# Kernel optimization log

Hardware: AMD Instinct MI355X
Metric: run time of the kernel (lower is better)

## Reference

```python
import jax, jax.numpy as jnp
import numpy as np

K = 512  # number of activations kept per row (init_kwargs k)


def setup_inputs() -> dict:
    key = jax.random.key(0)
    x = jax.random.normal(key, (8192, 8192), dtype=jnp.float32)
    return {"x": x}


def reference(x):
    # torch.topk(x, k, dim=1) -> indices of k largest per row
    _, idx = jax.lax.top_k(x, K)                      # idx: [B, K]
    rows = jnp.arange(x.shape[0])[:, None]            # [B, 1]
    # zeros_like + scatter(1, idx, 1)
    mask = jnp.zeros_like(x).at[rows, idx].set(1.0)   # [B, F]
    return x * mask
```

## Files before the change

### kernel.cpp

```cpp
#include <hip/hip_runtime.h>
#include <stdint.h>

#define FDIM 8192
#define KSEL 512
#define NT   512
#define EPT  (FDIM / NT / 4)

__device__ __forceinline__ unsigned keyOf(unsigned u) {
    return (u & 0x80000000u) ? ~u : (u | 0x80000000u);
}
__device__ __forceinline__ float valOf(unsigned key) {
    unsigned u = (key & 0x80000000u) ? (key ^ 0x80000000u) : ~key;
    return __uint_as_float(u);
}

__global__ __launch_bounds__(NT) void topk_mask_kernel(const float* __restrict__ x,
                                                       float* __restrict__ out) {
    __shared__ unsigned hist[256];
    __shared__ unsigned s_prefix, s_need, s_sub;
    __shared__ unsigned s_tiecnt;
    __shared__ unsigned tiebuf[64];

    const int row  = blockIdx.x;
    const int t    = threadIdx.x;
    const int lane = t & 63;

    const float4* xrow = (const float4*)(x + (size_t)row * FDIM);
    float4*       orow = (float4*)(out + (size_t)row * FDIM);

    uint4 kreg[EPT];
    #pragma unroll
    for (int j = 0; j < EPT; ++j) {
        float4 v = xrow[j * NT + t];
        kreg[j].x = keyOf(__float_as_uint(v.x));
        kreg[j].y = keyOf(__float_as_uint(v.y));
        kreg[j].z = keyOf(__float_as_uint(v.z));
        kreg[j].w = keyOf(__float_as_uint(v.w));
    }
    if (t < 256) hist[t] = 0u;
    if (t == 0) { s_prefix = 0u; s_need = KSEL; s_tiecnt = 0u; }
    __syncthreads();

    for (int round = 0; round < 4; ++round) {
        const int shift = 24 - 8 * round;
        const unsigned pref = s_prefix;

        if (round == 0) {
            #pragma unroll
            for (int j = 0; j < EPT; ++j) {
                #pragma unroll
                for (int c = 0; c < 4; ++c) {
                    unsigned key = (&kreg[j].x)[c];
                    unsigned dig = key >> 24;
                    unsigned long long m = ~0ull;
                    #pragma unroll
                    for (int b = 0; b < 8; ++b) {
                        unsigned long long bb = __ballot((dig >> b) & 1u);
                        m &= ((dig >> b) & 1u) ? bb : ~bb;
                    }
                    if (lane == __ffsll((long long)m) - 1)
                        atomicAdd(&hist[dig], (unsigned)__popcll(m));
                }
            }
        } else {
            #pragma unroll
            for (int j = 0; j < EPT; ++j) {
                #pragma unroll
                for (int c = 0; c < 4; ++c) {
                    unsigned key = (&kreg[j].x)[c];
                    if ((key >> (shift + 8)) == pref)
                        atomicAdd(&hist[(key >> shift) & 255u], 1u);
                }
            }
        }
        __syncthreads();

        if (t < 64) {
            const unsigned need = s_need;
            unsigned h0 = hist[4 * lane + 0];
            unsigned h1 = hist[4 * lane + 1];
            unsigned h2 = hist[4 * lane + 2];
            unsigned h3 = hist[4 * lane + 3];
            hist[4 * lane + 0] = 0u;
            hist[4 * lane + 1] = 0u;
            hist[4 * lane + 2] = 0u;
            hist[4 * lane + 3] = 0u;
            unsigned tot = h0 + h1 + h2 + h3;
            unsigned T = tot;
            #pragma unroll
            for (int off = 1; off < 64; off <<= 1) {
                unsigned y = __shfl_down(T, off);
                T += (lane + off < 64) ? y : 0u;
            }
            const unsigned beyond = T - tot;
            unsigned S3 = beyond + h3;
            unsigned S2 = S3 + h2;
            unsigned S1 = S2 + h1;
            unsigned S0 = S1 + h0;
            if (S0 >= need && S0 - h0 < need) {
                s_prefix = (pref << 8) | (unsigned)(4 * lane + 0);
                s_need = need - (S0 - h0); s_sub = h0;
            }
            if (S1 >= need && S1 - h1 < need) {
                s_prefix = (pref << 8) | (unsigned)(4 * lane + 1);
                s_need = need - (S1 - h1); s_sub = h1;
            }
            if (S2 >= need && S2 - h2 < need) {
                s_prefix = (pref << 8) | (unsigned)(4 * lane + 2);
                s_need = need - (S2 - h2); s_sub = h2;
            }
            if (S3 >= need && S3 - h3 < need) {
                s_prefix = (pref << 8) | (unsigned)(4 * lane + 3);
                s_need = need - (S3 - h3); s_sub = h3;
            }
        }
        __syncthreads();
    }

    const unsigned thresh = s_prefix;
    const unsigned keepEq = s_need;
    const unsigned eqCnt  = s_sub;
    const bool simple = (eqCnt == keepEq);

    if (simple) {
        #pragma unroll
        for (int j = 0; j < EPT; ++j) {
            uint4 k = kreg[j];
            float4 o;
            o.x = (k.x >= thresh) ? valOf(k.x) : 0.0f;
            o.y = (k.y >= thresh) ? valOf(k.y) : 0.0f;
            o.z = (k.z >= thresh) ? valOf(k.z) : 0.0f;
            o.w = (k.w >= thresh) ? valOf(k.w) : 0.0f;
            orow[j * NT + t] = o;
        }
    } else {
        #pragma unroll
        for (int j = 0; j < EPT; ++j) {
            uint4 k = kreg[j];
            float4 o;
            o.x = (k.x > thresh) ? valOf(k.x) : 0.0f;
            o.y = (k.y > thresh) ? valOf(k.y) : 0.0f;
            o.z = (k.z > thresh) ? valOf(k.z) : 0.0f;
            o.w = (k.w > thresh) ? valOf(k.w) : 0.0f;
            orow[j * NT + t] = o;
        }
        #pragma unroll
        for (int j = 0; j < EPT; ++j) {
            #pragma unroll
            for (int c = 0; c < 4; ++c) {
                unsigned key = (&kreg[j].x)[c];
                if (key == thresh) {
                    unsigned slot = atomicAdd(&s_tiecnt, 1u);
                    if (slot < 64u) tiebuf[slot] = 4u * (unsigned)(j * NT + t) + (unsigned)c;
                }
            }
        }
        __syncthreads();
        if (t == 0) {
            const unsigned m = s_tiecnt;
            const float v = valOf(thresh);
            if (m <= 64u) {
                for (unsigned i = 0; i < m; ++i) {
                    unsigned idx = tiebuf[i], rank = 0;
                    for (unsigned q = 0; q < m; ++q) rank += (tiebuf[q] < idx);
                    if (rank < keepEq) out[(size_t)row * FDIM + idx] = v;
                }
            } else {
                unsigned c = 0;
                for (int i = 0; i < FDIM && c < keepEq; ++i) {
                    if (keyOf(__float_as_uint(x[(size_t)row * FDIM + i])) == thresh) {
                        out[(size_t)row * FDIM + i] = v; ++c;
                    }
                }
            }
        }
    }
}

extern "C" void kernel_launch(void* const* d_in, const int* in_sizes, int n_in,
                              void* d_out, int out_size, void* d_ws, size_t ws_size,
                              hipStream_t stream) {
    const float* x = (const float*)d_in[0];
    float* out = (float*)d_out;
    topk_mask_kernel<<<dim3(FDIM), dim3(NT), 0, stream>>>(x, out);
}
```

Baseline: 455.4 us.

## Use 12/12/8-bit radix select with 4096-bin histogram and block-wide scan

Replaces the four 8-bit radix-select passes with three passes of 12, 12 and 8 bits, backed by a 4096-bin shared-memory histogram. The first pass drops the 8-ballot warp-aggregation loop and uses plain LDS atomics, relying on the wider bin spread to keep contention low. The threshold search becomes a scan across the whole block: per-thread suffix sums over 8 bins, a wave shuffle scan, then a cross-wave combine through shared memory. This removes a histogram pass and the ballot overhead, at the cost of more histogram zeroing, an extra barrier per round and 16KB of LDS.

```diff
diff --git a/kernel.cpp b/kernel.cpp
--- a/kernel.cpp
+++ b/kernel.cpp
@@ -5,6 +5,8 @@
 #define KSEL 512
 #define NT   512
 #define EPT  (FDIM / NT / 4)
+#define NBIN 4096
+#define NWAVE (NT / 64)
 
 __device__ __forceinline__ unsigned keyOf(unsigned u) {
     return (u & 0x80000000u) ? ~u : (u | 0x80000000u);
@@ -16,14 +18,15 @@
 
 __global__ __launch_bounds__(NT) void topk_mask_kernel(const float* __restrict__ x,
                                                        float* __restrict__ out) {
-    __shared__ unsigned hist[256];
-    __shared__ unsigned s_prefix, s_need, s_sub;
-    __shared__ unsigned s_tiecnt;
+    __shared__ unsigned hist[NBIN];
+    __shared__ unsigned wtot[NWAVE];
+    __shared__ unsigned s_prefix, s_need, s_sub, s_tiecnt;
     __shared__ unsigned tiebuf[64];
 
     const int row  = blockIdx.x;
     const int t    = threadIdx.x;
     const int lane = t & 63;
+    const int wave = t >> 6;
 
     const float4* xrow = (const float4*)(x + (size_t)row * FDIM);
     float4*       orow = (float4*)(out + (size_t)row * FDIM);
@@ -37,13 +40,15 @@
         kreg[j].z = keyOf(__float_as_uint(v.z));
         kreg[j].w = keyOf(__float_as_uint(v.w));
     }
-    if (t < 256) hist[t] = 0u;
+    #pragma unroll
+    for (int i = t; i < NBIN; i += NT) hist[i] = 0u;
     if (t == 0) { s_prefix = 0u; s_need = KSEL; s_tiecnt = 0u; }
     __syncthreads();
 
-    for (int round = 0; round < 4; ++round) {
-        const int shift = 24 - 8 * round;
+    #pragma unroll
+    for (int round = 0; round < 3; ++round) {
         const unsigned pref = s_prefix;
+        const unsigned need = s_need;
 
         if (round == 0) {
             #pragma unroll
@@ -51,15 +56,17 @@
                 #pragma unroll
                 for (int c = 0; c < 4; ++c) {
                     unsigned key = (&kreg[j].x)[c];
-                    unsigned dig = key >> 24;
-                    unsigned long long m = ~0ull;
-                    #pragma unroll
-                    for (int b = 0; b < 8; ++b) {
-                        unsigned long long bb = __ballot((dig >> b) & 1u);
-                        m &= ((dig >> b) & 1u) ? bb : ~bb;
-                    }
-                    if (lane == __ffsll((long long)m) - 1)
-                        atomicAdd(&hist[dig], (unsigned)__popcll(m));
+                    atomicAdd(&hist[key >> 20], 1u);
+                }
+            }
+        } else if (round == 1) {
+            #pragma unroll
+            for (int j = 0; j < EPT; ++j) {
+                #pragma unroll
+                for (int c = 0; c < 4; ++c) {
+                    unsigned key = (&kreg[j].x)[c];
+                    if ((key >> 20) == pref)
+                        atomicAdd(&hist[(key >> 8) & 0xFFFu], 1u);
                 }
             }
         } else {
@@ -68,50 +75,42 @@
                 #pragma unroll
                 for (int c = 0; c < 4; ++c) {
                     unsigned key = (&kreg[j].x)[c];
-                    if ((key >> (shift + 8)) == pref)
-                        atomicAdd(&hist[(key >> shift) & 255u], 1u);
+                    if ((key >> 8) == pref)
+                        atomicAdd(&hist[key & 0xFFu], 1u);
                 }
             }
         }
         __syncthreads();
 
-        if (t < 64) {
-            const unsigned need = s_need;
-            unsigned h0 = hist[4 * lane + 0];
-            unsigned h1 = hist[4 * lane + 1];
-            unsigned h2 = hist[4 * lane + 2];
-            unsigned h3 = hist[4 * lane + 3];
-            hist[4 * lane + 0] = 0u;
-            hist[4 * lane + 1] = 0u;
-            hist[4 * lane + 2] = 0u;
-            hist[4 * lane + 3] = 0u;
-            unsigned tot = h0 + h1 + h2 + h3;
-            unsigned T = tot;
-            #pragma unroll
-            for (int off = 1; off < 64; off <<= 1) {
-                unsigned y = __shfl_down(T, off);
-                T += (lane + off < 64) ? y : 0u;
-            }
-            const unsigned beyond = T - tot;
-            unsigned S3 = beyond + h3;
-            unsigned S2 = S3 + h2;
-            unsigned S1 = S2 + h1;
-            unsigned S0 = S1 + h0;
-            if (S0 >= need && S0 - h0 < need) {
-                s_prefix = (pref << 8) | (unsigned)(4 * lane + 0);
-                s_need = need - (S0 - h0); s_sub = h0;
-            }
-            if (S1 >= need && S1 - h1 < need) {
-                s_prefix = (pref << 8) | (unsigned)(4 * lane + 1);
-                s_need = need - (S1 - h1); s_sub = h1;
-            }
-            if (S2 >= need && S2 - h2 < need) {
-                s_prefix = (pref << 8) | (unsigned)(4 * lane + 2);
-                s_need = need - (S2 - h2); s_sub = h2;
-            }
-            if (S3 >= need && S3 - h3 < need) {
-                s_prefix = (pref << 8) | (unsigned)(4 * lane + 3);
-                s_need = need - (S3 - h3); s_sub = h3;
+        const unsigned base = (unsigned)t * (NBIN / NT);
+        unsigned sfx[9];
+        sfx[8] = 0u;
+        #pragma unroll
+        for (int i = 7; i >= 0; --i) sfx[i] = sfx[i + 1] + hist[base + i];
+        #pragma unroll
+        for (int i = 0; i < 8; ++i) hist[base + i] = 0u;
+        const unsigned tot = sfx[0];
+        unsigned incl = tot;
+        #pragma unroll
+        for (int off = 1; off < 64; off <<= 1) {
+            unsigned y = __shfl_down(incl, off);
+            incl += (lane + off < 64) ? y : 0u;
+        }
+        if (lane == 0) wtot[wave] = incl;
+        __syncthreads();
+        unsigned gb = incl - tot;
+        #pragma unroll
+        for (int w = 0; w < NWAVE; ++w) gb += (w > wave) ? wtot[w] : 0u;
+
+        #pragma unroll
+        for (int i = 0; i < 8; ++i) {
+            unsigned S = gb + sfx[i];
+            unsigned h = sfx[i] - sfx[i + 1];
+            if (S >= need && S - h < need) {
+                s_prefix = (round == 2) ? ((pref << 8) | (base + (unsigned)i))
+                                        : ((pref << 12) | (base + (unsigned)i));
+                s_need = need - (S - h);
+                s_sub  = h;
             }
         }
         __syncthreads();
```

Result: faster. 437.9 us (-3.8%).
